# Kernel optimization log

Hardware: AMD Instinct MI355X
Metric: run time of the kernel (lower is better)

Reference implementation:

```python
import jax, jax.numpy as jnp
import numpy as np

M, A, B, L = 3, 4, 2048, 7   # metapaths, instances-per-example, examples, path length (edges)
H = 256                       # hidden_size
V_N, V_E = 50000, 16          # node / edge vocab
EMB_RANGE = 14.0 / H          # gdel / hidden_size


def setup_inputs() -> dict:
    key = jax.random.key(0)
    ks = jax.random.split(key, 12)
    return {
        "tokens": jax.random.randint(ks[0], (M, A, B, L + 1), 0, V_N),
        "edge_tokens": jax.random.randint(ks[1], (M, A, B, L), 0, V_E),
        "node_emb": jax.random.uniform(ks[2], (V_N, H), minval=-EMB_RANGE, maxval=EMB_RANGE, dtype=jnp.float32),
        "edge_emb": jax.random.uniform(ks[3], (V_E, H // 2), minval=-EMB_RANGE, maxval=EMB_RANGE, dtype=jnp.float32),
        "scale_W": jax.random.normal(ks[4], (H, H), dtype=jnp.float32) * 0.05,
        "scale_b": jnp.zeros((H,), jnp.float32),
        "attn_W": jax.random.normal(ks[5], (2 * H, 2 * H), dtype=jnp.float32) * 0.05,
        "attn_b": jnp.zeros((2 * H,), jnp.float32),
        "intra_context": jax.random.uniform(ks[6], (2 * H,), dtype=jnp.float32),
        "inter_W": jax.random.normal(ks[7], (2 * H, 2 * H), dtype=jnp.float32) * 0.05,
        "inter_b": jnp.zeros((2 * H,), jnp.float32),
        "inter_context": jax.random.uniform(ks[8], (2 * H,), dtype=jnp.float32),
        "out_W": jax.random.normal(ks[9], (2 * H, H), dtype=jnp.float32) * 0.05,
        "out_b": jnp.zeros((H,), jnp.float32),
    }


def _forward(tokens, edge_tokens, node_emb, edge_emb, scale_W, scale_b,
             attn_W, attn_b, intra_context, inter_W, inter_b, inter_context,
             out_W, out_b):
    Mm, Aa, Bb, Lp1 = tokens.shape
    Ll = Lp1 - 1
    Hh = node_emb.shape[1]
    per_mp = []
    for m in range(Mm):                       # small fixed metapath count
        tok = tokens[m].reshape(-1, Lp1)      # [N, L+1], N = A*B
        etok = edge_tokens[m].reshape(-1, Ll) # [N, L]
        # embed_and_scale (dropout = identity at eval); one node type -> shared table/fc
        inputs = node_emb[tok] @ scale_W + scale_b   # [N, L+1, H]
        edge_in = edge_emb[etok]                     # [N, L, H/2]
        # rotational_encoding: reversed suffix scan with RotatE-style complex rotation
        hidden = inputs
        for i in reversed(range(Ll)):
            hr, hi = jnp.split(hidden[:, i + 1:, :], 2, axis=2)   # [N, L-i, H/2]
            ir, ii = jnp.split(inputs[:, i, :], 2, axis=1)        # [N, H/2]
            er = jnp.cos(edge_in[:, i])[:, None, :]
            ei = jnp.sin(edge_in[:, i])[:, None, :]
            out_r = ir[:, None, :] + er * hr - ei * hi
            out_i = ii[:, None, :] + ei * hr + er * hi
            hidden = hidden.at[:, i + 1:, :].set(jnp.concatenate([out_r, out_i], axis=2))
        path_lens = 1.0 + jnp.arange(Lp1, dtype=hidden.dtype)
        hidden = hidden / path_lens[None, :, None]
        # cat source node rep with each suffix rep -> [N, L, 2H]
        h_all = jnp.concatenate(
            [jnp.broadcast_to(hidden[:, :1, :], (hidden.shape[0], Ll, Hh)), hidden[:, 1:, :]],
            axis=2)
        # LstmAttn with use_rnn=False, full mask, static context
        act = jnp.tanh(h_all @ attn_W + attn_b)                   # [N, L, 2H]
        w = jax.nn.softmax(act @ intra_context, axis=1)           # [N, L]
        mh = jax.nn.relu(jnp.sum(h_all * w[:, :, None], axis=1))  # [N, 2H]
        per_mp.append(mh.reshape(Aa, Bb, 2 * Hh).sum(axis=0))     # [B, 2H]
    hid = jnp.stack(per_mp, axis=1)                               # [B, M, 2H]
    # inter-metapath attention: tanh(fc) averaged over batch, scored vs context
    h_act = jnp.tanh(hid @ inter_W + inter_b).mean(axis=0)        # [M, 2H]
    scores = h_act @ inter_context                                # [M]
    out = jnp.sum(hid * scores[None, :, None], axis=1)            # [B, 2H]
    return out @ out_W + out_b                                    # [B, H]


def reference(tokens, edge_tokens, node_emb, edge_emb, scale_W, scale_b,
              attn_W, attn_b, intra_context, inter_W, inter_b, inter_context,
              out_W, out_b):
    return _forward(tokens, edge_tokens, node_emb, edge_emb, scale_W, scale_b,
                    attn_W, attn_b, intra_context, inter_W, inter_b, inter_context,
                    out_W, out_b)
```

## Files before the change

kernel.cpp:

```cpp
#include <hip/hip_runtime.h>
#include <hip/hip_bf16.h>

typedef __bf16 bf16;
typedef bf16 bf16x8 __attribute__((ext_vector_type(8)));
typedef float f32x4 __attribute__((ext_vector_type(4)));

#define MFMA16(a, b, c) __builtin_amdgcn_mfma_f32_16x16x32_bf16((a), (b), (c), 0, 0, 0)

#define MM 3
#define AA 4
#define BB 2048
#define LL 7
#define HH 256
#define VN 50000

__device__ __forceinline__ float ftanh(float x) {
    float e = __expf(2.f * x);
    float r = __builtin_amdgcn_rcpf(e + 1.f);
    return 1.f - 2.f * r;
}
__device__ __forceinline__ float bf2f(unsigned u) {
    union { unsigned u; float f; } x; x.u = u << 16; return x.f;
}
__device__ __forceinline__ unsigned f2bf(float f) {
    bf16 b = (bf16)f;
    return (unsigned)__builtin_bit_cast(unsigned short, b);
}

__global__ void prep_kernel(const float* __restrict__ scale_W, const float* __restrict__ attn_W,
                            const float* __restrict__ inter_W, const float* __restrict__ out_W,
                            const float* __restrict__ edge_emb,
                            bf16* __restrict__ scale_WT, bf16* __restrict__ WtopT,
                            bf16* __restrict__ WbotT, bf16* __restrict__ inter_WT,
                            bf16* __restrict__ out_WT,
                            float* __restrict__ ce, float* __restrict__ se,
                            float* __restrict__ S) {
    int idx = blockIdx.x * blockDim.x + threadIdx.x;
    int stride = gridDim.x * blockDim.x;
    for (int i = idx; i < 256 * 256; i += stride) {
        int k = i >> 8, c = i & 255;
        scale_WT[c * 256 + k] = (bf16)scale_W[i];
    }
    for (int i = idx; i < 512 * 256; i += stride) {
        int c = i >> 8, k = i & 255;
        WtopT[c * 256 + k] = (bf16)attn_W[k * 512 + c];
        WbotT[c * 256 + k] = (bf16)attn_W[(256 + k) * 512 + c];
    }
    for (int i = idx; i < 512 * 512; i += stride) {
        int k = i >> 9, c = i & 511;
        inter_WT[c * 512 + k] = (bf16)inter_W[i];
    }
    for (int i = idx; i < 512 * 256; i += stride) {
        int k = i >> 8, c = i & 255;
        out_WT[c * 512 + k] = (bf16)out_W[i];
    }
    for (int i = idx; i < 16 * 128; i += stride) {
        float e = edge_emb[i];
        ce[i] = cosf(e);
        se[i] = sinf(e);
    }
    for (int i = idx; i < 3 * 512; i += stride) S[i] = 0.f;
}

__global__ __launch_bounds__(512, 4) void emb_gemm_kernel(
    const float* __restrict__ node_emb, const bf16* __restrict__ scale_WT,
    const float* __restrict__ scale_b, bf16* __restrict__ scaled_emb) {
    extern __shared__ char smem[];
    bf16* Al = (bf16*)smem;
    const int tid = threadIdx.x;
    const int vb = blockIdx.x * 64;
    const int w = tid >> 6, l = tid & 63, lr = l & 15, g = l >> 4;

    bf16x8 wf[8][2];
#pragma unroll
    for (int ks = 0; ks < 8; ++ks)
#pragma unroll
        for (int ct = 0; ct < 2; ++ct)
            wf[ks][ct] = *(const bf16x8*)(scale_WT + (size_t)(w * 32 + ct * 16 + lr) * 256 +
                                          ks * 32 + g * 8);
    float bia[2];
#pragma unroll
    for (int ct = 0; ct < 2; ++ct) bia[ct] = scale_b[w * 32 + ct * 16 + lr];

    for (int it = 0; it < 8; ++it) {
        int i = tid + it * 512;
        int r = i >> 6, kq = i & 63;
        int v = vb + r;
        float4 x = (v < VN) ? *(const float4*)(node_emb + (size_t)v * 256 + kq * 4)
                            : make_float4(0.f, 0.f, 0.f, 0.f);
        bf16* d = Al + r * 264 + kq * 4;
        d[0] = (bf16)x.x; d[1] = (bf16)x.y; d[2] = (bf16)x.z; d[3] = (bf16)x.w;
    }
    __syncthreads();

    for (int rt = 0; rt < 4; ++rt) {
        f32x4 acc[2] = {};
#pragma unroll
        for (int ks = 0; ks < 8; ++ks) {
            bf16x8 aF = *(const bf16x8*)(Al + (rt * 16 + lr) * 264 + ks * 32 + g * 8);
#pragma unroll
            for (int ct = 0; ct < 2; ++ct) acc[ct] = MFMA16(aF, wf[ks][ct], acc[ct]);
        }
#pragma unroll
        for (int ct = 0; ct < 2; ++ct) {
            int col = w * 32 + ct * 16 + lr;
#pragma unroll
            for (int i2 = 0; i2 < 4; ++i2) {
                int v = vb + rt * 16 + g * 4 + i2;
                if (v < VN) scaled_emb[(size_t)v * 256 + col] = (bf16)(acc[ct][i2] + bia[ct]);
            }
        }
    }
}

__global__ __launch_bounds__(256) void scan_kernel(
    const int* __restrict__ tokens, const int* __restrict__ etok,
    const bf16* __restrict__ scaled_emb, const float* __restrict__ ce,
    const float* __restrict__ se, bf16* __restrict__ scanned, int m0) {
    const int tid = threadIdx.x;
    const int n_l = blockIdx.x * 4 + (tid >> 6);
    const int cp = tid & 63, c0 = cp * 2;
    const int b = n_l & 2047, a = (n_l >> 11) & 3, mrel = n_l >> 13;
    const int base = ((m0 + mrel) * AA + a) * BB + b;
    const int* tk = tokens + (base << 3);
    const int* eb = etok + base * LL;
    bf16* orow = scanned + (size_t)n_l * 2048;

    unsigned x0r = *(const unsigned*)(scaled_emb + (size_t)tk[0] * 256 + c0);
    unsigned x0i = *(const unsigned*)(scaled_emb + (size_t)tk[0] * 256 + c0 + 128);
    *(unsigned*)(orow + c0) = x0r;
    *(unsigned*)(orow + c0 + 128) = x0i;
    float Sr0 = bf2f(x0r & 0xffffu), Sr1 = bf2f(x0r >> 16);
    float Si0 = bf2f(x0i & 0xffffu), Si1 = bf2f(x0i >> 16);
    float P0r = 1.f, P0i = 0.f, P1r = 1.f, P1i = 0.f;
#pragma unroll
    for (int k = 1; k <= LL; ++k) {
        int e = eb[k - 1];
        int v = tk[k];
        float2 crv = *(const float2*)(ce + e * 128 + c0);
        float2 civ = *(const float2*)(se + e * 128 + c0);
        float t0r = P0r * crv.x - P0i * civ.x, t0i = P0r * civ.x + P0i * crv.x;
        float t1r = P1r * crv.y - P1i * civ.y, t1i = P1r * civ.y + P1i * crv.y;
        P0r = t0r; P0i = t0i; P1r = t1r; P1i = t1i;
        unsigned xr = *(const unsigned*)(scaled_emb + (size_t)v * 256 + c0);
        unsigned xi = *(const unsigned*)(scaled_emb + (size_t)v * 256 + c0 + 128);
        float xr0 = bf2f(xr & 0xffffu), xr1 = bf2f(xr >> 16);
        float xi0 = bf2f(xi & 0xffffu), xi1 = bf2f(xi >> 16);
        Sr0 += P0r * xr0 - P0i * xi0; Si0 += P0r * xi0 + P0i * xr0;
        Sr1 += P1r * xr1 - P1i * xi1; Si1 += P1r * xi1 + P1i * xr1;
        float inv = 1.f / (float)(k + 1);
        *(unsigned*)(orow + k * 256 + c0) = f2bf(Sr0 * inv) | (f2bf(Sr1 * inv) << 16);
        *(unsigned*)(orow + k * 256 + c0 + 128) = f2bf(Si0 * inv) | (f2bf(Si1 * inv) << 16);
    }
}

__global__ __launch_bounds__(512, 4) void attn_kernel(
    const bf16* __restrict__ scanned, const bf16* __restrict__ WtopT,
    const bf16* __restrict__ WbotT, const float* __restrict__ attn_b,
    const float* __restrict__ ctx, float* __restrict__ hid, int m0) {
    extern __shared__ char smem[];
    bf16* Als = (bf16*)smem;
    bf16* h0l = (bf16*)(smem + 65536);
    float* lg2 = (float*)(smem + 73984);
    const int tid = threadIdx.x;
    const int w = tid >> 6, l = tid & 63, lr = l & 15, g = l >> 4;
    const int bg = blockIdx.x;
    const int mrel = bg >> 9;
    const int b0 = (bg & 511) * 4;
    const int m = m0 + mrel;

    for (int it = 0; it < 8; ++it) {
        int i = tid + it * 512;
        int row = i >> 5, Lch = i & 31;
        int q = row >> 3, p = row & 7;
        int a = q >> 2, bi = q & 3;
        const bf16* rp = scanned + ((size_t)(mrel * AA + a) * BB + b0 + bi) * 2048 + p * 256;
        bf16x8 x = *(const bf16x8*)(rp + Lch * 8);
        int pch = (Lch & 24) | ((Lch & 7) ^ p);
        *(bf16x8*)(Als + row * 256 + pch * 8) = x;
        if (p == 0) *(bf16x8*)(h0l + q * 264 + Lch * 8) = x;
    }
    __syncthreads();

    const int bsel = g >> 1;
    float pv[8][4] = {};
#pragma unroll 1
    for (int cc = 0; cc < 4; ++cc) {
        const int cb = cc * 128 + w * 16;
        f32x4 a0 = {};
        {
            bf16x8 wt[8];
#pragma unroll
            for (int ks = 0; ks < 8; ++ks)
                wt[ks] = *(const bf16x8*)(WtopT + (size_t)(cb + lr) * 256 + ks * 32 + g * 8);
#pragma unroll
            for (int ks = 0; ks < 8; ++ks) {
                bf16x8 aF = *(const bf16x8*)(h0l + lr * 264 + ks * 32 + g * 8);
                a0 = MFMA16(aF, wt[ks], a0);
            }
        }
        float y0sel[8];
#pragma unroll
        for (int rt = 0; rt < 8; ++rt) {
            float t0 = __shfl(a0[(2 * rt) & 3], (((2 * rt) >> 2) << 4) + lr, 64);
            float t1 = __shfl(a0[(2 * rt + 1) & 3], (((2 * rt + 1) >> 2) << 4) + lr, 64);
            y0sel[rt] = bsel ? t1 : t0;
        }
        bf16x8 wb[8];
#pragma unroll
        for (int ks = 0; ks < 8; ++ks)
            wb[ks] = *(const bf16x8*)(WbotT + (size_t)(cb + lr) * 256 + ks * 32 + g * 8);
        float bia = attn_b[cb + lr];
        float cxv = ctx[cb + lr];
#pragma unroll
        for (int rt = 0; rt < 8; ++rt) {
            float y0v = y0sel[rt];
            f32x4 accE, accO;
            accE[0] = y0v; accE[1] = y0v; accE[2] = y0v; accE[3] = y0v;
            accO[0] = 0.f; accO[1] = 0.f; accO[2] = 0.f; accO[3] = 0.f;
            __builtin_amdgcn_s_setprio(1);
#pragma unroll
            for (int ks = 0; ks < 4; ++ks) {
                bf16x8 aE = *(const bf16x8*)(Als + (rt * 16 + lr) * 256 +
                                             ((((2 * ks) * 4 + g) ^ (lr & 7)) << 3));
                bf16x8 aO = *(const bf16x8*)(Als + (rt * 16 + lr) * 256 +
                                             ((((2 * ks + 1) * 4 + g) ^ (lr & 7)) << 3));
                accE = MFMA16(aE, wb[2 * ks], accE);
                accO = MFMA16(aO, wb[2 * ks + 1], accO);
            }
            __builtin_amdgcn_s_setprio(0);
#pragma unroll
            for (int i2 = 0; i2 < 4; ++i2)
                pv[rt][i2] += cxv * ftanh(accE[i2] + accO[i2] + bia);
        }
        __builtin_amdgcn_sched_barrier(0);
    }
#pragma unroll
    for (int msk = 1; msk < 16; msk <<= 1)
#pragma unroll
        for (int rt = 0; rt < 8; ++rt)
#pragma unroll
            for (int i2 = 0; i2 < 4; ++i2) pv[rt][i2] += __shfl_xor(pv[rt][i2], msk, 64);
    if (lr == 0) {
#pragma unroll
        for (int rt = 0; rt < 8; ++rt)
#pragma unroll
            for (int i2 = 0; i2 < 4; ++i2) {
                int row = rt * 16 + g * 4 + i2;
                if (row & 7) lg2[row * 9 + w] = pv[rt][i2];
            }
    }
    __syncthreads();

    if (tid < 16) {
        int q = tid;
        float lv[LL], mx = -1e30f;
#pragma unroll
        for (int j = 1; j <= LL; ++j) {
            float sv = 0.f;
#pragma unroll
            for (int w8 = 0; w8 < 8; ++w8) sv += lg2[(q * 8 + j) * 9 + w8];
            lv[j - 1] = sv;
            mx = fmaxf(mx, sv);
        }
        float ssum = 0.f, ev[LL];
#pragma unroll
        for (int j = 0; j < LL; ++j) { ev[j] = __expf(lv[j] - mx); ssum += ev[j]; }
        float inv = 1.f / ssum;
#pragma unroll
        for (int j = 0; j < LL; ++j) lg2[(q * 8 + j + 1) * 9 + 8] = ev[j] * inv;
    }
    __syncthreads();

    for (int it2 = 0; it2 < 2; ++it2) {
        int item = tid + it2 * 512;
        int bi = item >> 8, cp = item & 255;
        int c0 = cp * 2;
        float acc0 = 0.f, acc1 = 0.f;
        if (c0 < 256) {
#pragma unroll
            for (int a = 0; a < AA; ++a) {
                int q = a * 4 + bi;
                unsigned u = *(const unsigned*)(Als + q * 2048 + c0);
                acc0 += fmaxf(0.f, bf2f(u & 0xffffu));
                acc1 += fmaxf(0.f, bf2f(u >> 16));
            }
        } else {
            int cb2 = c0 - 256;
            int ch = cb2 >> 3, of = cb2 & 7;
#pragma unroll
            for (int a = 0; a < AA; ++a) {
                int q = a * 4 + bi;
                float s0 = 0.f, s1 = 0.f;
#pragma unroll
                for (int j = 1; j <= LL; ++j) {
                    unsigned u = *(const unsigned*)(Als + (q * 8 + j) * 256 +
                                                    ((ch ^ j) << 3) + of);
                    float wj = lg2[(q * 8 + j) * 9 + 8];
                    s0 += wj * bf2f(u & 0xffffu);
                    s1 += wj * bf2f(u >> 16);
                }
                acc0 += fmaxf(0.f, s0);
                acc1 += fmaxf(0.f, s1);
            }
        }
        float2 o; o.x = acc0; o.y = acc1;
        *(float2*)(hid + ((size_t)(b0 + bi) * 3 + m) * 512 + c0) = o;
    }
}

__global__ __launch_bounds__(1024, 4) void inter_kernel(
    const float* __restrict__ hid, const bf16* __restrict__ inter_WT,
    const float* __restrict__ inter_b, float* __restrict__ S) {
    extern __shared__ char smem[];
    bf16* Al = (bf16*)smem;
    const int tid = threadIdx.x;
    const int m = blockIdx.y, rb = blockIdx.x * 32;
    const int w = tid >> 6, l = tid & 63, lr = l & 15, g = l >> 4;
    for (int it = 0; it < 4; ++it) {
        int i = tid + it * 1024;
        int r = i >> 7, kq = i & 127;
        float4 x = *(const float4*)(hid + ((size_t)(rb + r) * 3 + m) * 512 + kq * 4);
        bf16* d = Al + r * 520 + kq * 4;
        d[0] = (bf16)x.x; d[1] = (bf16)x.y; d[2] = (bf16)x.z; d[3] = (bf16)x.w;
    }
    __syncthreads();
#pragma unroll 1
    for (int cc = 0; cc < 2; ++cc) {
        int c = cc * 256 + w * 16 + lr;
        bf16x8 wf[16];
#pragma unroll
        for (int ks = 0; ks < 16; ++ks)
            wf[ks] = *(const bf16x8*)(inter_WT + (size_t)c * 512 + ks * 32 + g * 8);
        float biav = inter_b[c];
        float csum = 0.f;
        for (int rt = 0; rt < 2; ++rt) {
            f32x4 acc = {};
#pragma unroll
            for (int ks = 0; ks < 16; ++ks) {
                bf16x8 aF = *(const bf16x8*)(Al + (rt * 16 + lr) * 520 + ks * 32 + g * 8);
                acc = MFMA16(aF, wf[ks], acc);
            }
#pragma unroll
            for (int i2 = 0; i2 < 4; ++i2) csum += ftanh(acc[i2] + biav);
        }
        csum += __shfl_xor(csum, 16, 64);
        csum += __shfl_xor(csum, 32, 64);
        if (g == 0) atomicAdd(&S[m * 512 + c], csum);
        __builtin_amdgcn_sched_barrier(0);
    }
}

__global__ void scores_kernel(const float* __restrict__ S, const float* __restrict__ ictx2,
                              float* __restrict__ scores) {
    __shared__ float red[512];
    int t = threadIdx.x;
    for (int m = 0; m < 3; ++m) {
        red[t] = S[m * 512 + t] * ictx2[t];
        __syncthreads();
        for (int st = 256; st > 0; st >>= 1) {
            if (t < st) red[t] += red[t + st];
            __syncthreads();
        }
        if (t == 0) scores[m] = red[0] * (1.f / 2048.f);
        __syncthreads();
    }
}

__global__ __launch_bounds__(1024, 4) void out_kernel(
    const float* __restrict__ hid, const float* __restrict__ scores,
    const bf16* __restrict__ out_WT, const float* __restrict__ out_b,
    float* __restrict__ out) {
    extern __shared__ char smem[];
    bf16* Al = (bf16*)smem;
    const int tid = threadIdx.x;
    const int rb = blockIdx.x * 32;
    const int w = tid >> 6, l = tid & 63, lr = l & 15, g = l >> 4;
    float s0 = scores[0], s1 = scores[1], s2 = scores[2];
    for (int it = 0; it < 4; ++it) {
        int i = tid + it * 1024;
        int r = i >> 7, kq = i & 127;
        const float* hp = hid + (size_t)(rb + r) * 1536 + kq * 4;
        float4 x0 = *(const float4*)(hp);
        float4 x1 = *(const float4*)(hp + 512);
        float4 x2 = *(const float4*)(hp + 1024);
        bf16* d = Al + r * 520 + kq * 4;
        d[0] = (bf16)(x0.x * s0 + x1.x * s1 + x2.x * s2);
        d[1] = (bf16)(x0.y * s0 + x1.y * s1 + x2.y * s2);
        d[2] = (bf16)(x0.z * s0 + x1.z * s1 + x2.z * s2);
        d[3] = (bf16)(x0.w * s0 + x1.w * s1 + x2.w * s2);
    }
    __syncthreads();
    int c = w * 16 + lr;
    bf16x8 wf[16];
#pragma unroll
    for (int ks = 0; ks < 16; ++ks)
        wf[ks] = *(const bf16x8*)(out_WT + (size_t)c * 512 + ks * 32 + g * 8);
    float biav = out_b[c];
    for (int rt = 0; rt < 2; ++rt) {
        f32x4 acc = {};
#pragma unroll
        for (int ks = 0; ks < 16; ++ks) {
            bf16x8 aF = *(const bf16x8*)(Al + (rt * 16 + lr) * 520 + ks * 32 + g * 8);
            acc = MFMA16(aF, wf[ks], acc);
        }
#pragma unroll
        for (int i2 = 0; i2 < 4; ++i2)
            out[(size_t)(rb + rt * 16 + g * 4 + i2) * 256 + c] = acc[i2] + biav;
    }
}

extern "C" void kernel_launch(void* const* d_in, const int* in_sizes, int n_in,
                              void* d_out, int out_size, void* d_ws, size_t ws_size,
                              hipStream_t stream) {
    const int* tokens = (const int*)d_in[0];
    const int* etok = (const int*)d_in[1];
    const float* node_emb = (const float*)d_in[2];
    const float* edge_emb = (const float*)d_in[3];
    const float* scale_W = (const float*)d_in[4];
    const float* scale_b = (const float*)d_in[5];
    const float* attn_W = (const float*)d_in[6];
    const float* attn_b = (const float*)d_in[7];
    const float* ictx = (const float*)d_in[8];
    const float* inter_W = (const float*)d_in[9];
    const float* inter_b = (const float*)d_in[10];
    const float* ictx2 = (const float*)d_in[11];
    const float* out_W = (const float*)d_in[12];
    const float* out_b = (const float*)d_in[13];
    float* out = (float*)d_out;
    char* ws = (char*)d_ws;

    size_t off = 0;
    bf16* scale_WT = (bf16*)(ws + off); off += 256 * 256 * 2;
    bf16* WtopT = (bf16*)(ws + off);    off += 512 * 256 * 2;
    bf16* WbotT = (bf16*)(ws + off);    off += 512 * 256 * 2;
    bf16* inter_WT = (bf16*)(ws + off); off += 512 * 512 * 2;
    bf16* out_WT = (bf16*)(ws + off);   off += 512 * 256 * 2;
    float* ce = (float*)(ws + off);     off += 16 * 128 * 4;
    float* se = (float*)(ws + off);     off += 16 * 128 * 4;
    float* S = (float*)(ws + off);      off += 3 * 512 * 4;
    float* scores = (float*)(ws + off); off += 256;
    bf16* scaled_emb = (bf16*)(ws + off); off += (size_t)VN * 256 * 2;
    float* hid = (float*)(ws + off);    off += (size_t)BB * 3 * 512 * 4;
    bf16* scanned = (bf16*)(ws + off);
    const size_t chunk_bytes = (size_t)8192 * 8 * 256 * 2;
    size_t need3 = off + chunk_bytes;
    size_t need1 = off + 3 * chunk_bytes;
    if (ws_size < need3) return;
    const int nm = (ws_size >= need1) ? 3 : 1;

    const int lds_k1 = 64 * 264 * 2;
    const int lds_B = 78592;
    const int lds_k4 = 32 * 520 * 2;
    (void)hipFuncSetAttribute((const void*)attn_kernel,
                              hipFuncAttributeMaxDynamicSharedMemorySize, lds_B);

    prep_kernel<<<1024, 256, 0, stream>>>(scale_W, attn_W, inter_W, out_W, edge_emb,
                                          scale_WT, WtopT, WbotT, inter_WT, out_WT, ce, se, S);
    emb_gemm_kernel<<<(VN + 63) / 64, 512, lds_k1, stream>>>(node_emb, scale_WT, scale_b,
                                                             scaled_emb);
    for (int m0 = 0; m0 < 3; m0 += nm) {
        scan_kernel<<<nm * 2048, 256, 0, stream>>>(tokens, etok, scaled_emb, ce, se,
                                                   scanned, m0);
        attn_kernel<<<nm * 512, 512, lds_B, stream>>>(scanned, WtopT, WbotT, attn_b, ictx,
                                                      hid, m0);
    }
    inter_kernel<<<dim3(BB / 32, MM), 1024, lds_k4, stream>>>(hid, inter_WT, inter_b, S);
    scores_kernel<<<1, 512, 0, stream>>>(S, ictx2, scores);
    out_kernel<<<BB / 32, 1024, lds_k4, stream>>>(hid, scores, out_WT, out_b, out);
}
```

Before: 218.5 us.

## Fuse rotational scan into attention kernel, writing scanned rows directly to LDS

Moves the RotatE suffix scan out of its own kernel and into the prologue of the attention kernel, where each wave computes two instances and stores the scanned bf16 rows straight into the swizzled LDS tile. This removes the global round trip of the scanned tensor (about 100 MB written and read back) and one kernel launch per metapath chunk. The cost is that the scan now runs with the attention kernel's occupancy and sits serially ahead of the MFMA work in each block, with gathers from the embedding table exposed in that prologue.

```diff
diff --git a/kernel.cpp b/kernel.cpp
--- a/kernel.cpp
+++ b/kernel.cpp
@@ -113,51 +113,12 @@
     }
 }
 
-__global__ __launch_bounds__(256) void scan_kernel(
+__global__ __launch_bounds__(512, 4) void attn_kernel(
     const int* __restrict__ tokens, const int* __restrict__ etok,
-    const bf16* __restrict__ scaled_emb, const float* __restrict__ ce,
-    const float* __restrict__ se, bf16* __restrict__ scanned, int m0) {
-    const int tid = threadIdx.x;
-    const int n_l = blockIdx.x * 4 + (tid >> 6);
-    const int cp = tid & 63, c0 = cp * 2;
-    const int b = n_l & 2047, a = (n_l >> 11) & 3, mrel = n_l >> 13;
-    const int base = ((m0 + mrel) * AA + a) * BB + b;
-    const int* tk = tokens + (base << 3);
-    const int* eb = etok + base * LL;
-    bf16* orow = scanned + (size_t)n_l * 2048;
-
-    unsigned x0r = *(const unsigned*)(scaled_emb + (size_t)tk[0] * 256 + c0);
-    unsigned x0i = *(const unsigned*)(scaled_emb + (size_t)tk[0] * 256 + c0 + 128);
-    *(unsigned*)(orow + c0) = x0r;
-    *(unsigned*)(orow + c0 + 128) = x0i;
-    float Sr0 = bf2f(x0r & 0xffffu), Sr1 = bf2f(x0r >> 16);
-    float Si0 = bf2f(x0i & 0xffffu), Si1 = bf2f(x0i >> 16);
-    float P0r = 1.f, P0i = 0.f, P1r = 1.f, P1i = 0.f;
-#pragma unroll
-    for (int k = 1; k <= LL; ++k) {
-        int e = eb[k - 1];
-        int v = tk[k];
-        float2 crv = *(const float2*)(ce + e * 128 + c0);
-        float2 civ = *(const float2*)(se + e * 128 + c0);
-        float t0r = P0r * crv.x - P0i * civ.x, t0i = P0r * civ.x + P0i * crv.x;
-        float t1r = P1r * crv.y - P1i * civ.y, t1i = P1r * civ.y + P1i * crv.y;
-        P0r = t0r; P0i = t0i; P1r = t1r; P1i = t1i;
-        unsigned xr = *(const unsigned*)(scaled_emb + (size_t)v * 256 + c0);
-        unsigned xi = *(const unsigned*)(scaled_emb + (size_t)v * 256 + c0 + 128);
-        float xr0 = bf2f(xr & 0xffffu), xr1 = bf2f(xr >> 16);
-        float xi0 = bf2f(xi & 0xffffu), xi1 = bf2f(xi >> 16);
-        Sr0 += P0r * xr0 - P0i * xi0; Si0 += P0r * xi0 + P0i * xr0;
-        Sr1 += P1r * xr1 - P1i * xi1; Si1 += P1r * xi1 + P1i * xr1;
-        float inv = 1.f / (float)(k + 1);
-        *(unsigned*)(orow + k * 256 + c0) = f2bf(Sr0 * inv) | (f2bf(Sr1 * inv) << 16);
-        *(unsigned*)(orow + k * 256 + c0 + 128) = f2bf(Si0 * inv) | (f2bf(Si1 * inv) << 16);
-    }
-}
-
-__global__ __launch_bounds__(512, 4) void attn_kernel(
-    const bf16* __restrict__ scanned, const bf16* __restrict__ WtopT,
+    const bf16* __restrict__ scaled_emb, const bf16* __restrict__ WtopT,
     const bf16* __restrict__ WbotT, const float* __restrict__ attn_b,
-    const float* __restrict__ ctx, float* __restrict__ hid, int m0) {
+    const float* __restrict__ ctx, const float* __restrict__ ce,
+    const float* __restrict__ se, float* __restrict__ hid) {
     extern __shared__ char smem[];
     bf16* Als = (bf16*)smem;
     bf16* h0l = (bf16*)(smem + 65536);
@@ -165,20 +126,52 @@
     const int tid = threadIdx.x;
     const int w = tid >> 6, l = tid & 63, lr = l & 15, g = l >> 4;
     const int bg = blockIdx.x;
-    const int mrel = bg >> 9;
+    const int m = bg >> 9;
     const int b0 = (bg & 511) * 4;
-    const int m = m0 + mrel;
-
-    for (int it = 0; it < 8; ++it) {
-        int i = tid + it * 512;
-        int row = i >> 5, Lch = i & 31;
-        int q = row >> 3, p = row & 7;
-        int a = q >> 2, bi = q & 3;
-        const bf16* rp = scanned + ((size_t)(mrel * AA + a) * BB + b0 + bi) * 2048 + p * 256;
-        bf16x8 x = *(const bf16x8*)(rp + Lch * 8);
-        int pch = (Lch & 24) | ((Lch & 7) ^ p);
-        *(bf16x8*)(Als + row * 256 + pch * 8) = x;
-        if (p == 0) *(bf16x8*)(h0l + q * 264 + Lch * 8) = x;
+
+    {
+        const int c0 = l * 2;
+        const int Lch = c0 >> 3, of = c0 & 7;
+#pragma unroll 1
+        for (int qq = 0; qq < 2; ++qq) {
+            int q = w * 2 + qq;
+            int a = q >> 2, bi = q & 3;
+            int base = (m * AA + a) * BB + b0 + bi;
+            const int* tk = tokens + (base << 3);
+            const int* eb = etok + base * LL;
+            bf16* arow = Als + (q * 8) * 256;
+            unsigned x0r = *(const unsigned*)(scaled_emb + (size_t)tk[0] * 256 + c0);
+            unsigned x0i = *(const unsigned*)(scaled_emb + (size_t)tk[0] * 256 + c0 + 128);
+            *(unsigned*)(arow + Lch * 8 + of) = x0r;
+            *(unsigned*)(arow + (Lch + 16) * 8 + of) = x0i;
+            *(unsigned*)(h0l + q * 264 + c0) = x0r;
+            *(unsigned*)(h0l + q * 264 + c0 + 128) = x0i;
+            float Sr0 = bf2f(x0r & 0xffffu), Sr1 = bf2f(x0r >> 16);
+            float Si0 = bf2f(x0i & 0xffffu), Si1 = bf2f(x0i >> 16);
+            float P0r = 1.f, P0i = 0.f, P1r = 1.f, P1i = 0.f;
+#pragma unroll
+            for (int k = 1; k <= LL; ++k) {
+                int e = eb[k - 1];
+                int v = tk[k];
+                float2 crv = *(const float2*)(ce + e * 128 + c0);
+                float2 civ = *(const float2*)(se + e * 128 + c0);
+                float t0r = P0r * crv.x - P0i * civ.x, t0i = P0r * civ.x + P0i * crv.x;
+                float t1r = P1r * crv.y - P1i * civ.y, t1i = P1r * civ.y + P1i * crv.y;
+                P0r = t0r; P0i = t0i; P1r = t1r; P1i = t1i;
+                unsigned xr = *(const unsigned*)(scaled_emb + (size_t)v * 256 + c0);
+                unsigned xi = *(const unsigned*)(scaled_emb + (size_t)v * 256 + c0 + 128);
+                float xr0 = bf2f(xr & 0xffffu), xr1 = bf2f(xr >> 16);
+                float xi0 = bf2f(xi & 0xffffu), xi1 = bf2f(xi >> 16);
+                Sr0 += P0r * xr0 - P0i * xi0; Si0 += P0r * xi0 + P0i * xr0;
+                Sr1 += P1r * xr1 - P1i * xi1; Si1 += P1r * xi1 + P1i * xr1;
+                float inv = 1.f / (float)(k + 1);
+                bf16* rowk = Als + (q * 8 + k) * 256;
+                *(unsigned*)(rowk + ((Lch ^ k) << 3) + of) =
+                    f2bf(Sr0 * inv) | (f2bf(Sr1 * inv) << 16);
+                *(unsigned*)(rowk + (((Lch + 16) ^ k) << 3) + of) =
+                    f2bf(Si0 * inv) | (f2bf(Si1 * inv) << 16);
+            }
+        }
     }
     __syncthreads();
 
@@ -442,12 +435,7 @@
     float* scores = (float*)(ws + off); off += 256;
     bf16* scaled_emb = (bf16*)(ws + off); off += (size_t)VN * 256 * 2;
     float* hid = (float*)(ws + off);    off += (size_t)BB * 3 * 512 * 4;
-    bf16* scanned = (bf16*)(ws + off);
-    const size_t chunk_bytes = (size_t)8192 * 8 * 256 * 2;
-    size_t need3 = off + chunk_bytes;
-    size_t need1 = off + 3 * chunk_bytes;
-    if (ws_size < need3) return;
-    const int nm = (ws_size >= need1) ? 3 : 1;
+    if (ws_size < off) return;
 
     const int lds_k1 = 64 * 264 * 2;
     const int lds_B = 78592;
@@ -459,12 +447,8 @@
                                           scale_WT, WtopT, WbotT, inter_WT, out_WT, ce, se, S);
     emb_gemm_kernel<<<(VN + 63) / 64, 512, lds_k1, stream>>>(node_emb, scale_WT, scale_b,
                                                              scaled_emb);
-    for (int m0 = 0; m0 < 3; m0 += nm) {
-        scan_kernel<<<nm * 2048, 256, 0, stream>>>(tokens, etok, scaled_emb, ce, se,
-                                                   scanned, m0);
-        attn_kernel<<<nm * 512, 512, lds_B, stream>>>(scanned, WtopT, WbotT, attn_b, ictx,
-                                                      hid, m0);
-    }
+    attn_kernel<<<3 * 512, 512, lds_B, stream>>>(tokens, etok, scaled_emb, WtopT, WbotT,
+                                                 attn_b, ictx, ce, se, hid);
     inter_kernel<<<dim3(BB / 32, MM), 1024, lds_k4, stream>>>(hid, inter_WT, inter_b, S);
     scores_kernel<<<1, 512, 0, stream>>>(S, ictx2, scores);
     out_kernel<<<BB / 32, 1024, lds_k4, stream>>>(hid, scores, out_WT, out_b, out);
```

New measurement: 198.5 us. -9.1%, faster.
